# Kernel optimization log

Hardware: AMD Instinct MI355X
Metric: run time of the kernel (lower is better)

Reference implementation:

```python
import jax, jax.numpy as jnp
import numpy as np

N = 8192        # batch_size == num nodes == num hyperedges
D = 512         # hidden_dim
H_HEADS = 8
HD = D // H_HEADS
TOP_K = 16
EPS = 1e-5      # LayerNorm eps


def setup_inputs() -> dict:
    key = jax.random.key(0)
    ks = jax.random.split(key, 10)
    def rn(k, shape, scale=0.02):
        return jax.random.normal(k, shape, dtype=jnp.float32) * scale
    return {
        "x0": jax.random.normal(ks[0], (N, D), dtype=jnp.float32),
        "x1": jax.random.normal(ks[1], (N, D), dtype=jnp.float32),
        # modality projections: Linear -> ReLU -> LayerNorm (per modality)
        "w_p0": rn(ks[2], (D, D)), "b_p0": jnp.zeros((D,), jnp.float32),
        "g0": jnp.ones((D,), jnp.float32), "beta0": jnp.zeros((D,), jnp.float32),
        "w_p1": rn(ks[3], (D, D)), "b_p1": jnp.zeros((D,), jnp.float32),
        "g1": jnp.ones((D,), jnp.float32), "beta1": jnp.zeros((D,), jnp.float32),
        # MultiheadAttention packed in-proj + out-proj
        "in_w": rn(ks[4], (3 * D, D)), "in_b": jnp.zeros((3 * D,), jnp.float32),
        "out_w": rn(ks[5], (D, D)), "out_b": jnp.zeros((D,), jnp.float32),
        # edge weight predictor MLP
        "ew_w1": rn(ks[6], (D // 2, D)), "ew_b1": jnp.zeros((D // 2,), jnp.float32),
        "ew_w2": rn(ks[7], (1, D // 2)), "ew_b2": jnp.zeros((1,), jnp.float32),
    }


def _layernorm(x, g, b):
    m = x.mean(-1, keepdims=True)
    v = ((x - m) ** 2).mean(-1, keepdims=True)
    return (x - m) * jax.lax.rsqrt(v + EPS) * g + b


def _forward(x0, x1, w_p0, b_p0, g0, beta0, w_p1, b_p1, g1, beta1,
             in_w, in_b, out_w, out_b, ew_w1, ew_b1, ew_w2, ew_b2):
    # per-modality projection: Linear -> ReLU -> LayerNorm
    p0 = _layernorm(jax.nn.relu(x0 @ w_p0.T + b_p0), g0, beta0)
    p1 = _layernorm(jax.nn.relu(x1 @ w_p1.T + b_p1), g1, beta1)
    seq = jnp.stack([p0, p1], axis=1)                       # [N, 2, D]
    # cross-modal MHA (self-attention over the 2 modality tokens)
    qkv = seq @ in_w.T + in_b                               # [N, 2, 3D]
    q, k, v = jnp.split(qkv, 3, axis=-1)
    q = q.reshape(N, 2, H_HEADS, HD)
    k = k.reshape(N, 2, H_HEADS, HD)
    v = v.reshape(N, 2, H_HEADS, HD)
    scores = jnp.einsum('bqhd,bkhd->bhqk', q, k) / jnp.sqrt(jnp.float32(HD))
    attn = jax.nn.softmax(scores, axis=-1)                  # [N, h, 2, 2]
    ctx = jnp.einsum('bhqk,bkhd->bqhd', attn, v).reshape(N, 2, D)
    attended = ctx @ out_w.T + out_b                        # [N, 2, D]
    fused = attended.mean(axis=1)                           # [N, D]
    # node-node attention similarity, row-softmax
    sim = jax.nn.softmax(fused @ fused.T, axis=1)           # [N, N]
    _, idx = jax.lax.top_k(sim, TOP_K)                      # [N, K]
    vals = jnp.take_along_axis(sim, idx, axis=1)            # [N, K]
    rows = jnp.arange(N)
    # H[i,i]=1 first, then H[neighbor, i] = sim[i, neighbor] (may overwrite diag)
    H = jnp.zeros((N, N), sim.dtype).at[rows, rows].set(1.0)
    H = H.at[idx, rows[:, None]].set(vals)
    colsum = H.sum(axis=0)
    H = H.at[rows, rows].set(jnp.where(colsum == 0, 1.0, H[rows, rows]))
    # edge weights
    hidden = jax.nn.relu(fused @ ew_w1.T + ew_b1)
    ew = jax.nn.sigmoid(hidden @ ew_w2.T + ew_b2)[:, 0]     # [N]
    ew = jnp.maximum(ew, 1e-8)
    return H, ew


def reference(x0, x1, w_p0, b_p0, g0, beta0, w_p1, b_p1, g1, beta1,
              in_w, in_b, out_w, out_b, ew_w1, ew_b1, ew_w2, ew_b2):
    return _forward(x0, x1, w_p0, b_p0, g0, beta0, w_p1, b_p1, g1, beta1,
                    in_w, in_b, out_w, out_b, ew_w1, ew_b1, ew_w2, ew_b2)
```

## Files before the change

### kernel.cpp

```cpp
#include <hip/hip_runtime.h>
#include <hip/hip_bf16.h>

#define NN 8192
#define DD 512

typedef unsigned short u16;
typedef __bf16 bf16_t;
typedef bf16_t bf16x8 __attribute__((ext_vector_type(8)));
typedef float f32x4 __attribute__((ext_vector_type(4)));

__device__ __forceinline__ float bf2f(u16 h) {
    union { unsigned u; float f; } v; v.u = ((unsigned)h) << 16; return v.f;
}
__device__ __forceinline__ float bflo(unsigned u) {
    union { unsigned u; float f; } v; v.u = u << 16; return v.f;
}
__device__ __forceinline__ float bfhi(unsigned u) {
    union { unsigned u; float f; } v; v.u = u & 0xFFFF0000u; return v.f;
}
__device__ __forceinline__ u16 f2bf(float f) {
    union { float f; unsigned u; } v; v.f = f;
    unsigned r = v.u + 0x7fffu + ((v.u >> 16) & 1u);
    return (u16)(r >> 16);
}

__global__ __launch_bounds__(256) void cvt7(
        const float* __restrict__ s0, u16* __restrict__ d0,
        const float* __restrict__ s1, u16* __restrict__ d1,
        const float* __restrict__ s2, u16* __restrict__ d2,
        const float* __restrict__ s3, u16* __restrict__ d3,
        const float* __restrict__ s4, u16* __restrict__ d4,
        const float* __restrict__ s5, u16* __restrict__ d5,
        const float* __restrict__ s6, u16* __restrict__ d6) {
    size_t v = ((size_t)blockIdx.x * 256 + threadIdx.x) * 8;
    const float* s; u16* d; size_t off;
    if (v < 4194304)      { s = s0; d = d0; off = v; }
    else if (v < 8388608) { s = s1; d = d1; off = v - 4194304; }
    else if (v < 8650752) { s = s2; d = d2; off = v - 8388608; }
    else if (v < 8912896) { s = s3; d = d3; off = v - 8650752; }
    else if (v < 9699328) { s = s4; d = d4; off = v - 8912896; }
    else if (v < 9961472) { s = s5; d = d5; off = v - 9699328; }
    else                  { s = s6; d = d6; off = v - 9961472; }
    float4 a = *(const float4*)(s + off);
    float4 b = *(const float4*)(s + off + 4);
    ushort4 o0 = make_ushort4(f2bf(a.x), f2bf(a.y), f2bf(a.z), f2bf(a.w));
    ushort4 o1 = make_ushort4(f2bf(b.x), f2bf(b.y), f2bf(b.z), f2bf(b.w));
    *(ushort4*)(d + off) = o0;
    *(ushort4*)(d + off + 4) = o1;
}

#define EPS_LDS 136
template<bool RELU, bool BIAS, bool SPLIT>
__global__ __launch_bounds__(256) void gemm_bt(const u16* __restrict__ A,
        const u16* __restrict__ B, const float* __restrict__ bias,
        const u16* __restrict__ B2, const float* __restrict__ bias2, int halfY,
        u16* __restrict__ C, int M, int Nc, int K) {
    __shared__ alignas(16) u16 Smem[2][16384];
    const int t = threadIdx.x;
    const int lane = t & 63;
    const int wave = t >> 6;
    const int wm = (wave >> 1) * 64;
    const int wn = (wave & 1) * 64;
    const int rowA = blockIdx.y * 128;
    const int rowB = blockIdx.x * 128;
    if (SPLIT && (int)blockIdx.y >= halfY) { B = B2; bias = bias2; }

    f32x4 acc[4][4] = {};
    const int mrow = lane & 15;
    const int kk = (lane >> 4) * 8;
    const int nt = K >> 6;

    auto STAGE = [&](int buf, int k0) {
        u16* As = Smem[buf];
        u16* Bs = Smem[buf] + 8192;
        #pragma unroll
        for (int r = 0; r < 4; ++r) {
            int chunk = r * 256 + t;
            const u16* srcA = A + (size_t)(rowA + (chunk >> 3)) * K + k0 + (chunk & 7) * 8;
            __builtin_amdgcn_global_load_lds(
                (const __attribute__((address_space(1))) void*)srcA,
                (__attribute__((address_space(3))) void*)(As + chunk * 8), 16, 0, 0);
            const u16* srcB = B + (size_t)(rowB + (chunk >> 3)) * K + k0 + (chunk & 7) * 8;
            __builtin_amdgcn_global_load_lds(
                (const __attribute__((address_space(1))) void*)srcB,
                (__attribute__((address_space(3))) void*)(Bs + chunk * 8), 16, 0, 0);
        }
    };

    STAGE(0, 0);
    __syncthreads();
    int cur = 0;
    for (int ti = 0; ti < nt; ++ti) {
        if (ti + 1 < nt) STAGE(cur ^ 1, (ti + 1) << 6);
        const u16* As = Smem[cur];
        const u16* Bs = Smem[cur] + 8192;
        #pragma unroll
        for (int ks = 0; ks < 64; ks += 32) {
            bf16x8 af[4], bfv[4];
            #pragma unroll
            for (int i = 0; i < 4; ++i)
                af[i] = *(const bf16x8*)(As + (wm + i * 16 + mrow) * 64 + ks + kk);
            #pragma unroll
            for (int j = 0; j < 4; ++j)
                bfv[j] = *(const bf16x8*)(Bs + (wn + j * 16 + mrow) * 64 + ks + kk);
            #pragma unroll
            for (int i = 0; i < 4; ++i)
                #pragma unroll
                for (int j = 0; j < 4; ++j)
                    acc[i][j] = __builtin_amdgcn_mfma_f32_16x16x32_bf16(af[i], bfv[j], acc[i][j], 0, 0, 0);
        }
        __syncthreads();
        cur ^= 1;
    }

    u16* Ep = &Smem[0][0];
    const int er0 = wm + (lane >> 4) * 4;
    const int ec0 = wn + (lane & 15);
    #pragma unroll
    for (int j = 0; j < 4; ++j) {
        int c = ec0 + j * 16;
        float bv = BIAS ? bias[rowB + c] : 0.0f;
        #pragma unroll
        for (int i = 0; i < 4; ++i) {
            #pragma unroll
            for (int r = 0; r < 4; ++r) {
                float v = acc[i][j][r] + bv;
                if (RELU) v = fmaxf(v, 0.0f);
                Ep[(er0 + i * 16 + r) * EPS_LDS + c] = f2bf(v);
            }
        }
    }
    __syncthreads();
    #pragma unroll
    for (int pass = 0; pass < 8; ++pass) {
        int chunk = pass * 256 + t;
        int rloc = chunk >> 4, coff = (chunk & 15) * 8;
        bf16x8 v = *(const bf16x8*)(Ep + rloc * EPS_LDS + coff);
        *(bf16x8*)(C + (size_t)(rowA + rloc) * Nc + rowB + coff) = v;
    }
}

__global__ __launch_bounds__(256) void gemm_qkv(const u16* __restrict__ A,
        const u16* __restrict__ B, const float* __restrict__ bias,
        u16* __restrict__ V, float* __restrict__ scores) {
    __shared__ alignas(16) u16 Smem[128 * 64 * 2];
    u16* As = Smem;
    u16* Bs = Smem + 128 * 64;
    const int t = threadIdx.x;
    const int lane = t & 63;
    const int wave = t >> 6;
    const int wm = (wave >> 1) * 64;
    const int wn = (wave & 1) * 64;
    const int c = blockIdx.x;
    const int rowA = blockIdx.y * 128;
    const bool isQK = (c < 8);

    f32x4 acc[4][4] = {};
    const int mrow = lane & 15;
    const int kk = (lane >> 4) * 8;

    for (int k0 = 0; k0 < DD; k0 += 64) {
        __syncthreads();
        #pragma unroll
        for (int r = 0; r < 4; ++r) {
            int chunk = r * 256 + t;
            int rr = chunk >> 3;
            int brow = isQK ? (c * 64 + rr + ((rr >= 64) ? 448 : 0))
                            : (1024 + (c - 8) * 128 + rr);
            const u16* srcA = A + (size_t)(rowA + rr) * DD + k0 + (chunk & 7) * 8;
            __builtin_amdgcn_global_load_lds(
                (const __attribute__((address_space(1))) void*)srcA,
                (__attribute__((address_space(3))) void*)(As + chunk * 8), 16, 0, 0);
            const u16* srcB = B + (size_t)brow * DD + k0 + (chunk & 7) * 8;
            __builtin_amdgcn_global_load_lds(
                (const __attribute__((address_space(1))) void*)srcB,
                (__attribute__((address_space(3))) void*)(Bs + chunk * 8), 16, 0, 0);
        }
        __syncthreads();
        #pragma unroll
        for (int ks = 0; ks < 64; ks += 32) {
            bf16x8 af[4], bfv[4];
            #pragma unroll
            for (int i = 0; i < 4; ++i)
                af[i] = *(const bf16x8*)(As + (wm + i * 16 + mrow) * 64 + ks + kk);
            #pragma unroll
            for (int j = 0; j < 4; ++j)
                bfv[j] = *(const bf16x8*)(Bs + (wn + j * 16 + mrow) * 64 + ks + kk);
            #pragma unroll
            for (int i = 0; i < 4; ++i)
                #pragma unroll
                for (int j = 0; j < 4; ++j)
                    acc[i][j] = __builtin_amdgcn_mfma_f32_16x16x32_bf16(af[i], bfv[j], acc[i][j], 0, 0, 0);
        }
    }

    __syncthreads();
    const int lr0 = (lane >> 4) * 4;
    const int ec0 = wn + (lane & 15);
    #pragma unroll
    for (int h = 0; h < 2; ++h) {
        if ((wave >> 1) == h) {
            #pragma unroll
            for (int j = 0; j < 4; ++j) {
                int cc = ec0 + j * 16;
                int bcol = isQK ? ((cc < 64) ? c * 64 + cc : 448 + c * 64 + cc)
                                : (1024 + (c - 8) * 128 + cc);
                float bv = bias[bcol];
                #pragma unroll
                for (int i = 0; i < 4; ++i) {
                    #pragma unroll
                    for (int r = 0; r < 4; ++r)
                        Smem[(lr0 + i * 16 + r) * EPS_LDS + cc] = f2bf(acc[i][j][r] + bv);
                }
            }
        }
        __syncthreads();
        if (isQK) {
            if (t < 128) {
                int nd = t >> 2, cb = t & 3, tt2 = cb >> 1, ss = cb & 1;
                const u16* qrow = Smem + (2 * nd + tt2) * EPS_LDS;
                const u16* krow = Smem + (2 * nd + ss) * EPS_LDS + 64;
                float s = 0.0f;
                #pragma unroll
                for (int d8 = 0; d8 < 8; ++d8) {
                    bf16x8 qv = *(const bf16x8*)(qrow + d8 * 8);
                    bf16x8 kv = *(const bf16x8*)(krow + d8 * 8);
                    #pragma unroll
                    for (int u = 0; u < 8; ++u) s += (float)qv[u] * (float)kv[u];
                }
                scores[(size_t)(rowA / 2 + h * 32 + nd) * 32 + c * 4 + cb] = s * 0.125f;
            }
        } else {
            #pragma unroll
            for (int pass = 0; pass < 4; ++pass) {
                int chunk = pass * 256 + t;
                int rloc = chunk >> 4, coff = (chunk & 15) * 8;
                bf16x8 v = *(const bf16x8*)(Smem + rloc * EPS_LDS + coff);
                *(bf16x8*)(V + (size_t)(rowA + h * 64 + rloc) * 512 + (c - 8) * 128 + coff) = v;
            }
        }
        __syncthreads();
    }
}

#define SYM_LDS 129
__global__ __launch_bounds__(256) void gemm_symh(const u16* __restrict__ F,
        u16* __restrict__ C, const u16* __restrict__ W1,
        const float* __restrict__ b1, u16* __restrict__ Hid) {
    __shared__ alignas(16) u16 Smem[128 * SYM_LDS];
    const int bx = blockIdx.x, by = blockIdx.y;
    const bool isHid = (bx >= 64);
    if (!isHid && bx < by) return;
    u16* As = Smem;
    u16* Bs = Smem + 128 * 64;
    const int t = threadIdx.x;
    const int lane = t & 63;
    const int wave = t >> 6;
    const int wm = (wave >> 1) * 64;
    const int wn = (wave & 1) * 64;
    const int rowI = by * 128;
    const int rowJ = isHid ? (bx - 64) * 128 : bx * 128;
    const u16* Bsrc = isHid ? W1 : F;

    f32x4 acc[4][4] = {};
    const int mrow = lane & 15;
    const int kk = (lane >> 4) * 8;

    for (int k0 = 0; k0 < DD; k0 += 64) {
        __syncthreads();
        #pragma unroll
        for (int r = 0; r < 4; ++r) {
            int chunk = r * 256 + t;
            const u16* srcA = F + (size_t)(rowI + (chunk >> 3)) * DD + k0 + (chunk & 7) * 8;
            __builtin_amdgcn_global_load_lds(
                (const __attribute__((address_space(1))) void*)srcA,
                (__attribute__((address_space(3))) void*)(As + chunk * 8), 16, 0, 0);
            const u16* srcB = Bsrc + (size_t)(rowJ + (chunk >> 3)) * DD + k0 + (chunk & 7) * 8;
            __builtin_amdgcn_global_load_lds(
                (const __attribute__((address_space(1))) void*)srcB,
                (__attribute__((address_space(3))) void*)(Bs + chunk * 8), 16, 0, 0);
        }
        __syncthreads();
        #pragma unroll
        for (int ks = 0; ks < 64; ks += 32) {
            bf16x8 af[4], bfv[4];
            #pragma unroll
            for (int i = 0; i < 4; ++i)
                af[i] = *(const bf16x8*)(As + (wm + i * 16 + mrow) * 64 + ks + kk);
            #pragma unroll
            for (int j = 0; j < 4; ++j)
                bfv[j] = *(const bf16x8*)(Bs + (wn + j * 16 + mrow) * 64 + ks + kk);
            #pragma unroll
            for (int i = 0; i < 4; ++i)
                #pragma unroll
                for (int j = 0; j < 4; ++j)
                    acc[i][j] = __builtin_amdgcn_mfma_f32_16x16x32_bf16(af[i], bfv[j], acc[i][j], 0, 0, 0);
        }
    }

    __syncthreads();
    const int er0 = wm + (lane >> 4) * 4;
    const int ec0 = wn + (lane & 15);
    #pragma unroll
    for (int j = 0; j < 4; ++j) {
        int c = ec0 + j * 16;
        float bv = isHid ? b1[rowJ + c] : 0.0f;
        #pragma unroll
        for (int i = 0; i < 4; ++i) {
            #pragma unroll
            for (int r = 0; r < 4; ++r) {
                float v = acc[i][j][r] + bv;
                if (isHid) v = fmaxf(v, 0.0f);
                Smem[(er0 + i * 16 + r) * SYM_LDS + c] = f2bf(v);
            }
        }
    }
    __syncthreads();
    if (isHid) {
        #pragma unroll
        for (int pass = 0; pass < 8; ++pass) {
            int chunk = pass * 256 + t;
            int rloc = chunk >> 4, coff = (chunk & 15) * 8;
            union { u16 us[8]; bf16x8 v; } buf;
            #pragma unroll
            for (int k = 0; k < 8; ++k) buf.us[k] = Smem[rloc * SYM_LDS + coff + k];
            *(bf16x8*)(Hid + (size_t)(rowI + rloc) * 256 + rowJ + coff) = buf.v;
        }
        return;
    }
    #pragma unroll
    for (int pass = 0; pass < 8; ++pass) {
        int chunk = pass * 256 + t;
        int rloc = chunk >> 4, coff = (chunk & 15) * 8;
        union { u16 us[8]; bf16x8 v; } buf;
        #pragma unroll
        for (int k = 0; k < 8; ++k) buf.us[k] = Smem[rloc * SYM_LDS + coff + k];
        *(bf16x8*)(C + (size_t)(rowI + rloc) * NN + rowJ + coff) = buf.v;
    }
    if (bx != by) {
        #pragma unroll
        for (int pass = 0; pass < 8; ++pass) {
            int chunk = pass * 256 + t;
            int tr = chunk >> 4, roff = (chunk & 15) * 8;
            union { u16 us[8]; bf16x8 v; } buf;
            #pragma unroll
            for (int k = 0; k < 8; ++k) buf.us[k] = Smem[(roff + k) * SYM_LDS + tr];
            *(bf16x8*)(C + (size_t)(rowJ + tr) * NN + rowI + roff) = buf.v;
        }
    }
}

__global__ __launch_bounds__(256) void ln2_kernel(const u16* __restrict__ y,
        const float* __restrict__ g0, const float* __restrict__ b0,
        const float* __restrict__ g1, const float* __restrict__ b1,
        u16* __restrict__ seq) {
    int n = blockIdx.x * 4 + (threadIdx.x >> 6);
    int lane = threadIdx.x & 63;
    int modality = n >> 13, node = n & (NN - 1);
    const float* g = modality ? g1 : g0;
    const float* b = modality ? b1 : b0;
    bf16x8 v = *(const bf16x8*)(y + (size_t)n * DD + lane * 8);
    float x[8];
    float s = 0.0f;
    #pragma unroll
    for (int u = 0; u < 8; ++u) { x[u] = (float)v[u]; s += x[u]; }
    #pragma unroll
    for (int off = 32; off; off >>= 1) s += __shfl_xor(s, off);
    float mean = s * (1.0f / DD);
    float vs = 0.0f;
    #pragma unroll
    for (int u = 0; u < 8; ++u) { x[u] -= mean; vs += x[u] * x[u]; }
    #pragma unroll
    for (int off = 32; off; off >>= 1) vs += __shfl_xor(vs, off);
    float inv = rsqrtf(vs * (1.0f / DD) + 1e-5f);
    float4 ga = *(const float4*)(g + lane * 8);
    float4 gb = *(const float4*)(g + lane * 8 + 4);
    float4 ba = *(const float4*)(b + lane * 8);
    float4 bb = *(const float4*)(b + lane * 8 + 4);
    union { u16 us[8]; bf16x8 v; } o;
    o.us[0] = f2bf(x[0] * inv * ga.x + ba.x);
    o.us[1] = f2bf(x[1] * inv * ga.y + ba.y);
    o.us[2] = f2bf(x[2] * inv * ga.z + ba.z);
    o.us[3] = f2bf(x[3] * inv * ga.w + ba.w);
    o.us[4] = f2bf(x[4] * inv * gb.x + bb.x);
    o.us[5] = f2bf(x[5] * inv * gb.y + bb.y);
    o.us[6] = f2bf(x[6] * inv * gb.z + bb.z);
    o.us[7] = f2bf(x[7] * inv * gb.w + bb.w);
    *(bf16x8*)(seq + (size_t)node * (2 * DD) + modality * DD + lane * 8) = o.v;
}

__global__ __launch_bounds__(256) void attn_v(const float* __restrict__ scores,
        const u16* __restrict__ V, u16* __restrict__ ctxm) {
    int n = blockIdx.x * 4 + (threadIdx.x >> 6);
    int lane = threadIdx.x & 63;
    int h = lane >> 3;
    float4 sc = *(const float4*)(scores + (size_t)n * 32 + h * 4);
    float s00 = sc.x, s01 = sc.y, s10 = sc.z, s11 = sc.w;
    float m0 = fmaxf(s00, s01), e00 = __expf(s00 - m0), e01 = __expf(s01 - m0);
    float a00 = e00 / (e00 + e01), a01 = e01 / (e00 + e01);
    float m1 = fmaxf(s10, s11), e10 = __expf(s10 - m1), e11 = __expf(s11 - m1);
    float a10 = e10 / (e10 + e11), a11 = e11 / (e10 + e11);
    float al0 = 0.5f * (a00 + a10), al1 = 0.5f * (a01 + a11);
    bf16x8 v0 = *(const bf16x8*)(V + (size_t)(2 * n) * 512 + lane * 8);
    bf16x8 v1 = *(const bf16x8*)(V + (size_t)(2 * n + 1) * 512 + lane * 8);
    union { u16 us[8]; bf16x8 v; } o;
    #pragma unroll
    for (int u = 0; u < 8; ++u)
        o.us[u] = f2bf(al0 * (float)v0[u] + al1 * (float)v1[u]);
    *(bf16x8*)(ctxm + (size_t)n * 512 + lane * 8) = o.v;
}

__global__ __launch_bounds__(256) void topk_bf16(const u16* __restrict__ S,
        float* __restrict__ topv, int* __restrict__ topi) {
    const float NEG = -3e38f;
    int row = blockIdx.x * 4 + (threadIdx.x >> 6);
    int lane = threadIdx.x & 63;
    const u16* Sr = S + (size_t)row * NN;

    float m = NEG, l = 0.0f;
    float t1v = NEG, t2v = NEG;
    int t1i = 0x7FFFFFFF, t2i = 0x7FFFFFFF;

    #pragma unroll
    for (int p = 0; p < 16; ++p) {
        uint4 raw = *(const uint4*)(Sr + p * 512 + lane * 8);
        int base = p * 512 + lane * 8;
        #pragma unroll
        for (int q = 0; q < 4; ++q) {
            unsigned w = (&raw.x)[q];
            #pragma unroll
            for (int h = 0; h < 2; ++h) {
                float x = h ? bfhi(w) : bflo(w);
                int xi = base + q * 2 + h;
                if (x > m) { l = l * __expf(m - x) + 1.0f; m = x; }
                else l += __expf(x - m);
                bool g1 = x > t1v, g2 = x > t2v;
                t2v = g1 ? t1v : (g2 ? x : t2v);
                t2i = g1 ? t1i : (g2 ? xi : t2i);
                t1v = g1 ? x : t1v;
                t1i = g1 ? xi : t1i;
            }
        }
    }
    #pragma unroll
    for (int off = 32; off; off >>= 1) {
        float om = __shfl_xor(m, off);
        float ol = __shfl_xor(l, off);
        float nm = fmaxf(m, om);
        l = l * __expf(m - nm) + ol * __expf(om - nm);
        m = nm;
    }

    unsigned mk0 = 0, mk1 = 0, mk2 = 0, mk3 = 0;
    float cv = t1v; int ci = t1i;
    float bv = t2v; int bi = t2i;
    for (int r = 0; r < 16; ++r) {
        float wv = cv; int wi = ci;
        #pragma unroll
        for (int off = 32; off; off >>= 1) {
            float ov = __shfl_xor(wv, off);
            int oi = __shfl_xor(wi, off);
            if (ov > wv || (ov == wv && oi < wi)) { wv = ov; wi = oi; }
        }
        if (lane == 0) {
            topv[(size_t)row * 16 + r] = __expf(wv - m) / l;
            topi[(size_t)row * 16 + r] = wi;
        }
        if (wi == ci) {
            int slot = ((wi >> 9) << 3) | (wi & 7);
            unsigned bit = 1u << (slot & 31);
            if (slot < 32) mk0 |= bit; else if (slot < 64) mk1 |= bit;
            else if (slot < 96) mk2 |= bit; else mk3 |= bit;
            cv = bv; ci = bi;
            bv = NEG; bi = 0x7FFFFFFF;
            if (ci == 0x7FFFFFFF) {
                float nb = NEG; int ni = 0x7FFFFFFF;
                #pragma unroll
                for (int p = 0; p < 16; ++p) {
                    uint4 raw = *(const uint4*)(Sr + p * 512 + lane * 8);
                    int base = p * 512 + lane * 8;
                    #pragma unroll
                    for (int q = 0; q < 4; ++q) {
                        unsigned w = (&raw.x)[q];
                        #pragma unroll
                        for (int h = 0; h < 2; ++h) {
                            int sl = p * 8 + q * 2 + h;
                            unsigned mw = (sl < 32) ? mk0 : (sl < 64) ? mk1
                                        : (sl < 96) ? mk2 : mk3;
                            float x = ((mw >> (sl & 31)) & 1u) ? NEG
                                    : (h ? bfhi(w) : bflo(w));
                            if (x > nb) { nb = x; ni = base + q * 2 + h; }
                        }
                    }
                }
                cv = nb; ci = ni;
            }
        }
    }
}

__global__ __launch_bounds__(256) void scatter_diag(const float* __restrict__ topv,
        const int* __restrict__ topi, float* __restrict__ H) {
    int tk = blockIdx.x * 256 + threadIdx.x;
    if (tk < NN * 16) {
        int i = tk >> 4;
        int idx = topi[tk];
        H[(size_t)idx * NN + i] = topv[tk];
    } else {
        int c = tk - NN * 16;
        const int* ti = topi + c * 16;
        bool self = false;
        #pragma unroll
        for (int j = 0; j < 16; ++j) self |= (ti[j] == c);
        if (!self) H[(size_t)c * NN + c] = 1.0f;
    }
}

__global__ __launch_bounds__(256) void ew_kernel(const u16* __restrict__ hidden,
        const float* __restrict__ w2, const float* __restrict__ b2, float* __restrict__ out) {
    int n = blockIdx.x * 4 + (threadIdx.x >> 6);
    int lane = threadIdx.x & 63;
    const u16* hr = hidden + (size_t)n * 256;
    float s = 0.0f;
    #pragma unroll
    for (int p = 0; p < 4; ++p) s += bf2f(hr[lane + p * 64]) * w2[lane + p * 64];
    for (int off = 32; off; off >>= 1) s += __shfl_xor(s, off);
    if (lane == 0) {
        float z = s + b2[0];
        float sig = 1.0f / (1.0f + __expf(-z));
        out[n] = fmaxf(sig, 1e-8f);
    }
}

extern "C" void kernel_launch(void* const* d_in, const int* in_sizes, int n_in,
                              void* d_out, int out_size, void* d_ws, size_t ws_size,
                              hipStream_t stream) {
    const float* x0    = (const float*)d_in[0];
    const float* x1    = (const float*)d_in[1];
    const float* w_p0  = (const float*)d_in[2];
    const float* b_p0  = (const float*)d_in[3];
    const float* g0    = (const float*)d_in[4];
    const float* beta0 = (const float*)d_in[5];
    const float* w_p1  = (const float*)d_in[6];
    const float* b_p1  = (const float*)d_in[7];
    const float* g1    = (const float*)d_in[8];
    const float* beta1 = (const float*)d_in[9];
    const float* in_w  = (const float*)d_in[10];
    const float* in_b  = (const float*)d_in[11];
    const float* out_w = (const float*)d_in[12];
    const float* out_b = (const float*)d_in[13];
    const float* ew_w1 = (const float*)d_in[14];
    const float* ew_b1 = (const float*)d_in[15];
    const float* ew_w2 = (const float*)d_in[16];
    const float* ew_b2 = (const float*)d_in[17];

    float* Hf = (float*)d_out;
    float* ew_out = Hf + (size_t)NN * NN;

    u16* Hu = (u16*)d_out;
    u16* x0b    = Hu;
    u16* x1b    = Hu + 4194304;
    u16* y01    = Hu + 8388608;
    u16* seq    = Hu + 16777216;
    u16* Vbuf   = Hu + 25165824;
    u16* ctxm   = Hu + 50331648;
    u16* hidden = Hu + 54525952;
    float* scB  = (float*)(Hu + 58720256);
    u16* wp0b   = Hu + 60817408;
    u16* wp1b   = wp0b + 262144;
    u16* inwb   = wp1b + 262144;
    u16* outwb  = inwb + 786432;
    u16* eww1b  = outwb + 262144;
    u16* Sb     = Hu + 67108864;
    char* ws = (char*)d_ws;
    u16* fusedB = (u16*)ws;
    float* topv = (float*)(ws + (8u << 20));
    int*   topi = (int*)(ws + (8u << 20) + 524288);

    dim3 blk(256);
    const int BIG = 1 << 30;
    cvt7<<<dim3(4928), blk, 0, stream>>>(x0, x0b, x1, x1b, w_p0, wp0b, w_p1, wp1b,
                                         in_w, inwb, out_w, outwb, ew_w1, eww1b);
    gemm_bt<true, true, true><<<dim3(4, 128), blk, 0, stream>>>(
        x0b, wp0b, b_p0, wp1b, b_p1, 64, y01, 2 * NN, DD, DD);
    ln2_kernel<<<dim3(2 * NN / 4), blk, 0, stream>>>(y01, g0, beta0, g1, beta1, seq);
    gemm_qkv<<<dim3(12, 128), blk, 0, stream>>>(seq, inwb, in_b, Vbuf, scB);
    attn_v<<<dim3(NN / 4), blk, 0, stream>>>(scB, Vbuf, ctxm);
    gemm_bt<false, true, false><<<dim3(4, 64), blk, 0, stream>>>(
        ctxm, outwb, out_b, nullptr, nullptr, BIG, fusedB, NN, DD, DD);
    gemm_symh<<<dim3(66, 64), blk, 0, stream>>>(fusedB, Sb, eww1b, ew_b1, hidden);
    ew_kernel<<<dim3(NN / 4), blk, 0, stream>>>(hidden, ew_w2, ew_b2, ew_out);
    topk_bf16<<<dim3(NN / 4), blk, 0, stream>>>(Sb, topv, topi);
    hipMemsetAsync(Hf, 0, (size_t)NN * NN * sizeof(float), stream);
    scatter_diag<<<dim3((NN * 16 + NN) / 256), blk, 0, stream>>>(topv, topi, Hf);
}
```

Baseline: 656.4 us.

## Overlap H zero-fill with symmetric GEMM and top-k kernels, fold ew into top-k

Splits the zeroing of the 256 MB H output into three pieces. Extra blocks in the sim GEMM zero the first region, extra blocks in the top-k kernel zero a middle region, and a smaller memset clears the remaining half. The edge-weight kernel is merged into the top-k launch, whose extra blocks also clear the bf16 hidden scratch, which is likely aliased into H. The aim is to hide memory-bound fill work behind compute-bound GEMM and top-k scanning and to drop one launch, at the cost of fragile hardcoded offsets into aliased buffers.

New measurement: 684.5 us. +4.3%, slower.

```diff
diff --git a/kernel.cpp b/kernel.cpp
--- a/kernel.cpp
+++ b/kernel.cpp
@@ -246,14 +246,23 @@
 #define SYM_LDS 129
 __global__ __launch_bounds__(256) void gemm_symh(const u16* __restrict__ F,
         u16* __restrict__ C, const u16* __restrict__ W1,
-        const float* __restrict__ b1, u16* __restrict__ Hid) {
+        const float* __restrict__ b1, u16* __restrict__ Hid,
+        float* __restrict__ Hz) {
     __shared__ alignas(16) u16 Smem[128 * SYM_LDS];
     const int bx = blockIdx.x, by = blockIdx.y;
+    const int t = threadIdx.x;
+    if (bx >= 66) {
+        float* base = Hz + (size_t)((bx - 66) * 64 + by) * 106496;
+        float4 z = make_float4(0.f, 0.f, 0.f, 0.f);
+        #pragma unroll 4
+        for (int i = 0; i < 104; ++i)
+            *(float4*)(base + i * 1024 + t * 4) = z;
+        return;
+    }
     const bool isHid = (bx >= 64);
     if (!isHid && bx < by) return;
     u16* As = Smem;
     u16* Bs = Smem + 128 * 64;
-    const int t = threadIdx.x;
     const int lane = t & 63;
     const int wave = t >> 6;
     const int wm = (wave >> 1) * 64;
@@ -411,10 +420,46 @@
 }
 
 __global__ __launch_bounds__(256) void topk_bf16(const u16* __restrict__ S,
-        float* __restrict__ topv, int* __restrict__ topi) {
+        float* __restrict__ topv, int* __restrict__ topi,
+        float* __restrict__ Hz108, u16* __restrict__ hidden,
+        const float* __restrict__ w2, const float* __restrict__ b2,
+        float* __restrict__ ew_out) {
+    const int blk = blockIdx.x;
+    const int t = threadIdx.x;
+    if (blk >= 2112) {
+        int wave = t >> 6, lane = t & 63;
+        int n0 = (blk - 2112) * 64 + wave * 16;
+        float w = w2[lane] , wb = w2[lane + 64], wc = w2[lane + 128], wd = w2[lane + 192];
+        for (int q = 0; q < 16; ++q) {
+            int n = n0 + q;
+            const u16* hr = hidden + (size_t)n * 256;
+            float s = bf2f(hr[lane]) * w + bf2f(hr[lane + 64]) * wb
+                    + bf2f(hr[lane + 128]) * wc + bf2f(hr[lane + 192]) * wd;
+            #pragma unroll
+            for (int off = 32; off; off >>= 1) s += __shfl_xor(s, off);
+            if (lane == 0) {
+                float z = s + b2[0];
+                float sig = 1.0f / (1.0f + __expf(-z));
+                ew_out[n] = fmaxf(sig, 1e-8f);
+            }
+        }
+        float4 z = make_float4(0.f, 0.f, 0.f, 0.f);
+        float4* zb = (float4*)(hidden + (size_t)n0 * 256);
+        #pragma unroll
+        for (int i = 0; i < 8; ++i) zb[i * 64 + lane] = z;
+        return;
+    }
+    if (blk >= 2048) {
+        float* base = Hz108 + (size_t)(blk - 2048) * 81920;
+        float4 z = make_float4(0.f, 0.f, 0.f, 0.f);
+        #pragma unroll 4
+        for (int i = 0; i < 80; ++i)
+            *(float4*)(base + i * 1024 + t * 4) = z;
+        return;
+    }
     const float NEG = -3e38f;
-    int row = blockIdx.x * 4 + (threadIdx.x >> 6);
-    int lane = threadIdx.x & 63;
+    int row = blk * 4 + (t >> 6);
+    int lane = t & 63;
     const u16* Sr = S + (size_t)row * NN;
 
     float m = NEG, l = 0.0f;
@@ -516,22 +561,6 @@
     }
 }
 
-__global__ __launch_bounds__(256) void ew_kernel(const u16* __restrict__ hidden,
-        const float* __restrict__ w2, const float* __restrict__ b2, float* __restrict__ out) {
-    int n = blockIdx.x * 4 + (threadIdx.x >> 6);
-    int lane = threadIdx.x & 63;
-    const u16* hr = hidden + (size_t)n * 256;
-    float s = 0.0f;
-    #pragma unroll
-    for (int p = 0; p < 4; ++p) s += bf2f(hr[lane + p * 64]) * w2[lane + p * 64];
-    for (int off = 32; off; off >>= 1) s += __shfl_xor(s, off);
-    if (lane == 0) {
-        float z = s + b2[0];
-        float sig = 1.0f / (1.0f + __expf(-z));
-        out[n] = fmaxf(sig, 1e-8f);
-    }
-}
-
 extern "C" void kernel_launch(void* const* d_in, const int* in_sizes, int n_in,
                               void* d_out, int out_size, void* d_ws, size_t ws_size,
                               hipStream_t stream) {
@@ -588,9 +617,9 @@
     attn_v<<<dim3(NN / 4), blk, 0, stream>>>(scB, Vbuf, ctxm);
     gemm_bt<false, true, false><<<dim3(4, 64), blk, 0, stream>>>(
         ctxm, outwb, out_b, nullptr, nullptr, BIG, fusedB, NN, DD, DD);
-    gemm_symh<<<dim3(66, 64), blk, 0, stream>>>(fusedB, Sb, eww1b, ew_b1, hidden);
-    ew_kernel<<<dim3(NN / 4), blk, 0, stream>>>(hidden, ew_w2, ew_b2, ew_out);
-    topk_bf16<<<dim3(NN / 4), blk, 0, stream>>>(Sb, topv, topi);
-    hipMemsetAsync(Hf, 0, (size_t)NN * NN * sizeof(float), stream);
+    gemm_symh<<<dim3(70, 64), blk, 0, stream>>>(fusedB, Sb, eww1b, ew_b1, hidden, Hf);
+    topk_bf16<<<dim3(2240), blk, 0, stream>>>(Sb, topv, topi,
+        (float*)(Hu + 56623104), hidden, ew_w2, ew_b2, ew_out);
+    hipMemsetAsync(Hf + 33554432, 0, (size_t)134217728, stream);
     scatter_diag<<<dim3((NN * 16 + NN) / 256), blk, 0, stream>>>(topv, topi, Hf);
 }
```

## Double-buffer LDS in QKV and sym GEMMs, fuse edge-weight into top-k

Applied to the files above, without the earlier changes.

Both the QKV GEMM and the symmetric similarity GEMM now use two LDS buffers, so the global-to-LDS load of the next K tile is issued while MFMAs run on the current one. This removes one barrier per iteration and overlaps memory latency with compute. The QKV epilogue now writes the whole 128-row tile in a single pass instead of two halves, which cuts barriers. The separate edge-weight kernel is folded into extra blocks of the top-k launch to save one launch. LDS use per block grows to 64KB, which can lower occupancy.

Measured after the change: 624.3 us. -4.9%, faster.

```diff
diff --git a/kernel.cpp b/kernel.cpp
--- a/kernel.cpp
+++ b/kernel.cpp
@@ -143,9 +143,7 @@
 __global__ __launch_bounds__(256) void gemm_qkv(const u16* __restrict__ A,
         const u16* __restrict__ B, const float* __restrict__ bias,
         u16* __restrict__ V, float* __restrict__ scores) {
-    __shared__ alignas(16) u16 Smem[128 * 64 * 2];
-    u16* As = Smem;
-    u16* Bs = Smem + 128 * 64;
+    __shared__ alignas(16) u16 Smem[2][16384];
     const int t = threadIdx.x;
     const int lane = t & 63;
     const int wave = t >> 6;
@@ -159,8 +157,9 @@
     const int mrow = lane & 15;
     const int kk = (lane >> 4) * 8;
 
-    for (int k0 = 0; k0 < DD; k0 += 64) {
-        __syncthreads();
+    auto STAGE = [&](int buf, int k0) {
+        u16* As = Smem[buf];
+        u16* Bs = Smem[buf] + 8192;
         #pragma unroll
         for (int r = 0; r < 4; ++r) {
             int chunk = r * 256 + t;
@@ -176,7 +175,15 @@
                 (const __attribute__((address_space(1))) void*)srcB,
                 (__attribute__((address_space(3))) void*)(Bs + chunk * 8), 16, 0, 0);
         }
-        __syncthreads();
+    };
+
+    STAGE(0, 0);
+    __syncthreads();
+    int cur = 0;
+    for (int ti = 0; ti < 8; ++ti) {
+        if (ti + 1 < 8) STAGE(cur ^ 1, (ti + 1) << 6);
+        const u16* As = Smem[cur];
+        const u16* Bs = Smem[cur] + 8192;
         #pragma unroll
         for (int ks = 0; ks < 64; ks += 32) {
             bf16x8 af[4], bfv[4];
@@ -192,54 +199,48 @@
                 for (int j = 0; j < 4; ++j)
                     acc[i][j] = __builtin_amdgcn_mfma_f32_16x16x32_bf16(af[i], bfv[j], acc[i][j], 0, 0, 0);
         }
-    }
-
+        __syncthreads();
+        cur ^= 1;
+    }
+
+    u16* Ep = &Smem[0][0];
+    const int er0 = wm + (lane >> 4) * 4;
+    const int ec0 = wn + (lane & 15);
+    #pragma unroll
+    for (int j = 0; j < 4; ++j) {
+        int cc = ec0 + j * 16;
+        int bcol = isQK ? ((cc < 64) ? c * 64 + cc : 448 + c * 64 + cc)
+                        : (1024 + (c - 8) * 128 + cc);
+        float bv = bias[bcol];
+        #pragma unroll
+        for (int i = 0; i < 4; ++i) {
+            #pragma unroll
+            for (int r = 0; r < 4; ++r)
+                Ep[(er0 + i * 16 + r) * EPS_LDS + cc] = f2bf(acc[i][j][r] + bv);
+        }
+    }
     __syncthreads();
-    const int lr0 = (lane >> 4) * 4;
-    const int ec0 = wn + (lane & 15);
-    #pragma unroll
-    for (int h = 0; h < 2; ++h) {
-        if ((wave >> 1) == h) {
-            #pragma unroll
-            for (int j = 0; j < 4; ++j) {
-                int cc = ec0 + j * 16;
-                int bcol = isQK ? ((cc < 64) ? c * 64 + cc : 448 + c * 64 + cc)
-                                : (1024 + (c - 8) * 128 + cc);
-                float bv = bias[bcol];
-                #pragma unroll
-                for (int i = 0; i < 4; ++i) {
-                    #pragma unroll
-                    for (int r = 0; r < 4; ++r)
-                        Smem[(lr0 + i * 16 + r) * EPS_LDS + cc] = f2bf(acc[i][j][r] + bv);
-                }
-            }
-        }
-        __syncthreads();
-        if (isQK) {
-            if (t < 128) {
-                int nd = t >> 2, cb = t & 3, tt2 = cb >> 1, ss = cb & 1;
-                const u16* qrow = Smem + (2 * nd + tt2) * EPS_LDS;
-                const u16* krow = Smem + (2 * nd + ss) * EPS_LDS + 64;
-                float s = 0.0f;
-                #pragma unroll
-                for (int d8 = 0; d8 < 8; ++d8) {
-                    bf16x8 qv = *(const bf16x8*)(qrow + d8 * 8);
-                    bf16x8 kv = *(const bf16x8*)(krow + d8 * 8);
-                    #pragma unroll
-                    for (int u = 0; u < 8; ++u) s += (float)qv[u] * (float)kv[u];
-                }
-                scores[(size_t)(rowA / 2 + h * 32 + nd) * 32 + c * 4 + cb] = s * 0.125f;
-            }
-        } else {
-            #pragma unroll
-            for (int pass = 0; pass < 4; ++pass) {
-                int chunk = pass * 256 + t;
-                int rloc = chunk >> 4, coff = (chunk & 15) * 8;
-                bf16x8 v = *(const bf16x8*)(Smem + rloc * EPS_LDS + coff);
-                *(bf16x8*)(V + (size_t)(rowA + h * 64 + rloc) * 512 + (c - 8) * 128 + coff) = v;
-            }
-        }
-        __syncthreads();
+    if (isQK) {
+        int nd = t >> 2, cb = t & 3, tt2 = cb >> 1, ss = cb & 1;
+        const u16* qrow = Ep + (2 * nd + tt2) * EPS_LDS;
+        const u16* krow = Ep + (2 * nd + ss) * EPS_LDS + 64;
+        float s = 0.0f;
+        #pragma unroll
+        for (int d8 = 0; d8 < 8; ++d8) {
+            bf16x8 qv = *(const bf16x8*)(qrow + d8 * 8);
+            bf16x8 kv = *(const bf16x8*)(krow + d8 * 8);
+            #pragma unroll
+            for (int u = 0; u < 8; ++u) s += (float)qv[u] * (float)kv[u];
+        }
+        scores[(size_t)(rowA / 2 + nd) * 32 + c * 4 + cb] = s * 0.125f;
+    } else {
+        #pragma unroll
+        for (int pass = 0; pass < 8; ++pass) {
+            int chunk = pass * 256 + t;
+            int rloc = chunk >> 4, coff = (chunk & 15) * 8;
+            bf16x8 v = *(const bf16x8*)(Ep + rloc * EPS_LDS + coff);
+            *(bf16x8*)(V + (size_t)(rowA + rloc) * 512 + (c - 8) * 128 + coff) = v;
+        }
     }
 }
 
@@ -247,12 +248,10 @@
 __global__ __launch_bounds__(256) void gemm_symh(const u16* __restrict__ F,
         u16* __restrict__ C, const u16* __restrict__ W1,
         const float* __restrict__ b1, u16* __restrict__ Hid) {
-    __shared__ alignas(16) u16 Smem[128 * SYM_LDS];
+    __shared__ alignas(16) u16 Smem[2][16384];
     const int bx = blockIdx.x, by = blockIdx.y;
     const bool isHid = (bx >= 64);
     if (!isHid && bx < by) return;
-    u16* As = Smem;
-    u16* Bs = Smem + 128 * 64;
     const int t = threadIdx.x;
     const int lane = t & 63;
     const int wave = t >> 6;
@@ -266,8 +265,9 @@
     const int mrow = lane & 15;
     const int kk = (lane >> 4) * 8;
 
-    for (int k0 = 0; k0 < DD; k0 += 64) {
-        __syncthreads();
+    auto STAGE = [&](int buf, int k0) {
+        u16* As = Smem[buf];
+        u16* Bs = Smem[buf] + 8192;
         #pragma unroll
         for (int r = 0; r < 4; ++r) {
             int chunk = r * 256 + t;
@@ -280,7 +280,15 @@
                 (const __attribute__((address_space(1))) void*)srcB,
                 (__attribute__((address_space(3))) void*)(Bs + chunk * 8), 16, 0, 0);
         }
-        __syncthreads();
+    };
+
+    STAGE(0, 0);
+    __syncthreads();
+    int cur = 0;
+    for (int ti = 0; ti < 8; ++ti) {
+        if (ti + 1 < 8) STAGE(cur ^ 1, (ti + 1) << 6);
+        const u16* As = Smem[cur];
+        const u16* Bs = Smem[cur] + 8192;
         #pragma unroll
         for (int ks = 0; ks < 64; ks += 32) {
             bf16x8 af[4], bfv[4];
@@ -296,9 +304,11 @@
                 for (int j = 0; j < 4; ++j)
                     acc[i][j] = __builtin_amdgcn_mfma_f32_16x16x32_bf16(af[i], bfv[j], acc[i][j], 0, 0, 0);
         }
-    }
-
-    __syncthreads();
+        __syncthreads();
+        cur ^= 1;
+    }
+
+    u16* Ep = &Smem[0][0];
     const int er0 = wm + (lane >> 4) * 4;
     const int ec0 = wn + (lane & 15);
     #pragma unroll
@@ -311,7 +321,7 @@
             for (int r = 0; r < 4; ++r) {
                 float v = acc[i][j][r] + bv;
                 if (isHid) v = fmaxf(v, 0.0f);
-                Smem[(er0 + i * 16 + r) * SYM_LDS + c] = f2bf(v);
+                Ep[(er0 + i * 16 + r) * SYM_LDS + c] = f2bf(v);
             }
         }
     }
@@ -323,7 +333,7 @@
             int rloc = chunk >> 4, coff = (chunk & 15) * 8;
             union { u16 us[8]; bf16x8 v; } buf;
             #pragma unroll
-            for (int k = 0; k < 8; ++k) buf.us[k] = Smem[rloc * SYM_LDS + coff + k];
+            for (int k = 0; k < 8; ++k) buf.us[k] = Ep[rloc * SYM_LDS + coff + k];
             *(bf16x8*)(Hid + (size_t)(rowI + rloc) * 256 + rowJ + coff) = buf.v;
         }
         return;
@@ -334,7 +344,7 @@
         int rloc = chunk >> 4, coff = (chunk & 15) * 8;
         union { u16 us[8]; bf16x8 v; } buf;
         #pragma unroll
-        for (int k = 0; k < 8; ++k) buf.us[k] = Smem[rloc * SYM_LDS + coff + k];
+        for (int k = 0; k < 8; ++k) buf.us[k] = Ep[rloc * SYM_LDS + coff + k];
         *(bf16x8*)(C + (size_t)(rowI + rloc) * NN + rowJ + coff) = buf.v;
     }
     if (bx != by) {
@@ -344,7 +354,7 @@
             int tr = chunk >> 4, roff = (chunk & 15) * 8;
             union { u16 us[8]; bf16x8 v; } buf;
             #pragma unroll
-            for (int k = 0; k < 8; ++k) buf.us[k] = Smem[(roff + k) * SYM_LDS + tr];
+            for (int k = 0; k < 8; ++k) buf.us[k] = Ep[(roff + k) * SYM_LDS + tr];
             *(bf16x8*)(C + (size_t)(rowJ + tr) * NN + rowI + roff) = buf.v;
         }
     }
@@ -411,10 +421,33 @@
 }
 
 __global__ __launch_bounds__(256) void topk_bf16(const u16* __restrict__ S,
-        float* __restrict__ topv, int* __restrict__ topi) {
+        float* __restrict__ topv, int* __restrict__ topi,
+        const u16* __restrict__ hidden, const float* __restrict__ w2,
+        const float* __restrict__ b2, float* __restrict__ ew_out) {
+    const int blk = blockIdx.x;
+    const int t = threadIdx.x;
+    if (blk >= 2048) {
+        int wv = t >> 6, lane = t & 63;
+        int n0 = (blk - 2048) * 64 + wv * 16;
+        float wa = w2[lane], wb = w2[lane + 64], wc = w2[lane + 128], wd = w2[lane + 192];
+        for (int q = 0; q < 16; ++q) {
+            int n = n0 + q;
+            const u16* hr = hidden + (size_t)n * 256;
+            float s = bf2f(hr[lane]) * wa + bf2f(hr[lane + 64]) * wb
+                    + bf2f(hr[lane + 128]) * wc + bf2f(hr[lane + 192]) * wd;
+            #pragma unroll
+            for (int off = 32; off; off >>= 1) s += __shfl_xor(s, off);
+            if (lane == 0) {
+                float z = s + b2[0];
+                float sig = 1.0f / (1.0f + __expf(-z));
+                ew_out[n] = fmaxf(sig, 1e-8f);
+            }
+        }
+        return;
+    }
     const float NEG = -3e38f;
-    int row = blockIdx.x * 4 + (threadIdx.x >> 6);
-    int lane = threadIdx.x & 63;
+    int row = blk * 4 + (t >> 6);
+    int lane = t & 63;
     const u16* Sr = S + (size_t)row * NN;
 
     float m = NEG, l = 0.0f;
@@ -516,22 +549,6 @@
     }
 }
 
-__global__ __launch_bounds__(256) void ew_kernel(const u16* __restrict__ hidden,
-        const float* __restrict__ w2, const float* __restrict__ b2, float* __restrict__ out) {
-    int n = blockIdx.x * 4 + (threadIdx.x >> 6);
-    int lane = threadIdx.x & 63;
-    const u16* hr = hidden + (size_t)n * 256;
-    float s = 0.0f;
-    #pragma unroll
-    for (int p = 0; p < 4; ++p) s += bf2f(hr[lane + p * 64]) * w2[lane + p * 64];
-    for (int off = 32; off; off >>= 1) s += __shfl_xor(s, off);
-    if (lane == 0) {
-        float z = s + b2[0];
-        float sig = 1.0f / (1.0f + __expf(-z));
-        out[n] = fmaxf(sig, 1e-8f);
-    }
-}
-
 extern "C" void kernel_launch(void* const* d_in, const int* in_sizes, int n_in,
                               void* d_out, int out_size, void* d_ws, size_t ws_size,
                               hipStream_t stream) {
@@ -589,8 +606,8 @@
     gemm_bt<false, true, false><<<dim3(4, 64), blk, 0, stream>>>(
         ctxm, outwb, out_b, nullptr, nullptr, BIG, fusedB, NN, DD, DD);
     gemm_symh<<<dim3(66, 64), blk, 0, stream>>>(fusedB, Sb, eww1b, ew_b1, hidden);
-    ew_kernel<<<dim3(NN / 4), blk, 0, stream>>>(hidden, ew_w2, ew_b2, ew_out);
-    topk_bf16<<<dim3(NN / 4), blk, 0, stream>>>(Sb, topv, topi);
+    topk_bf16<<<dim3(2176), blk, 0, stream>>>(Sb, topv, topi,
+        hidden, ew_w2, ew_b2, ew_out);
     hipMemsetAsync(Hf, 0, (size_t)NN * NN * sizeof(float), stream);
     scatter_diag<<<dim3((NN * 16 + NN) / 256), blk, 0, stream>>>(topv, topi, Hf);
 }
```
